# Kernel tuning notes

Measured on AMD Instinct MI355X. Metric: run time of the kernel, lower is better.

## Reference

```python
import jax, jax.numpy as jnp
import numpy as np

CLAMP = 10000.0
EPS = 1e-8
NUM_HEADS = 4


def _sanitize(t):
    t = jnp.nan_to_num(t, nan=0.0, posinf=CLAMP, neginf=-CLAMP)
    return jnp.clip(t, -CLAMP, CLAMP)


def _rmsnorm(t, w):
    # Matches the torch module: L2-norm based RMS, eps added OUTSIDE the sqrt.
    t = _sanitize(t)
    d = t.shape[-1]
    rms = jnp.linalg.norm(t, axis=-1, keepdims=True) * (1.0 / np.sqrt(float(d)))
    return w * (t / (rms + EPS))


def setup_inputs() -> dict:
    key = jax.random.key(0)
    ks = jax.random.split(key, 7)
    N, C, S = 100000, 1024, 18
    x = jax.random.normal(ks[0], (N, C), dtype=jnp.float32)
    seeds = jax.random.normal(ks[1], (S, C), dtype=jnp.float32) / np.sqrt(float(C))
    w_nq = jnp.ones((C,), dtype=jnp.float32)
    w_nkv = jnp.ones((C,), dtype=jnp.float32)
    # nn.MultiheadAttention params (xavier-ish scale)
    in_proj_w = jax.random.normal(ks[2], (3 * C, C), dtype=jnp.float32) * (1.0 / np.sqrt(float(C)))
    in_proj_b = jnp.zeros((3 * C,), dtype=jnp.float32)
    out_proj_w = jax.random.normal(ks[3], (C, C), dtype=jnp.float32) * (1.0 / np.sqrt(float(C)))
    out_proj_b = jnp.zeros((C,), dtype=jnp.float32)
    return {"x": x, "seeds": seeds, "w_nq": w_nq, "w_nkv": w_nkv,
            "in_proj_w": in_proj_w, "in_proj_b": in_proj_b,
            "out_proj_w": out_proj_w, "out_proj_b": out_proj_b}


def reference(x, seeds, w_nq, w_nkv, in_proj_w, in_proj_b, out_proj_w, out_proj_b):
    x = _sanitize(x)
    N, C = x.shape
    S = seeds.shape[0]
    H = NUM_HEADS
    Dh = C // H

    q = _rmsnorm(seeds, w_nq)      # (S, C)
    kv = _rmsnorm(x, w_nkv)        # (N, C) -- same tensor feeds both k and v

    Wq, Wk, Wv = in_proj_w[:C], in_proj_w[C:2 * C], in_proj_w[2 * C:]
    bq, bk, bv = in_proj_b[:C], in_proj_b[C:2 * C], in_proj_b[2 * C:]

    qp = (q @ Wq.T + bq).reshape(S, H, Dh) * (1.0 / np.sqrt(float(Dh)))
    kp = (kv @ Wk.T + bk).reshape(N, H, Dh)
    vp = (kv @ Wv.T + bv).reshape(N, H, Dh)

    # (H, S, N) scores -- S=18 << N, skinny attention
    scores = jnp.einsum('shd,nhd->hsn', qp, kp)
    attn = jax.nn.softmax(scores, axis=-1)
    o = jnp.einsum('hsn,nhd->shd', attn, vp).reshape(S, C)

    y = o @ out_proj_w.T + out_proj_b   # (S, C)
    ctx = _sanitize(y.mean(axis=0))     # (C,)
    return ctx
```

## Files before the change

### kernel.cpp

```cpp
#include <hip/hip_runtime.h>
#include <math.h>

#define NTOK 100000
#define C 1024
#define SN 18
#define H 4
#define DH 256
#define HSN 72
#define CLAMPV 10000.0f
#define EPSV 1e-8f

using short8 = __attribute__((ext_vector_type(8))) short;
using f32x4  = __attribute__((ext_vector_type(4))) float;

__device__ __forceinline__ float sanitize_f(float v) {
    if (isnan(v)) return 0.0f;
    return fminf(CLAMPV, fmaxf(-CLAMPV, v));
}
__device__ __forceinline__ unsigned short f2bf(float f) {
    unsigned int u = __float_as_uint(f);
    u = (u + 0x7FFFu + ((u >> 16) & 1u)) >> 16;
    return (unsigned short)u;
}
__device__ __forceinline__ float waveSum(float v) {
    #pragma unroll
    for (int o = 32; o > 0; o >>= 1) v += __shfl_down(v, o, 64);
    return v;
}
__device__ __forceinline__ float waveMax(float v) {
    #pragma unroll
    for (int o = 32; o > 0; o >>= 1) v = fmaxf(v, __shfl_down(v, o, 64));
    return v;
}

__global__ void k_qnorm(const float* __restrict__ seeds, const float* __restrict__ w_nq,
                        float* __restrict__ q) {
    int row = blockIdx.x, tid = threadIdx.x;
    const float* src = seeds + (size_t)row * C;
    float ss = 0.f;
    for (int c = tid; c < C; c += 256) { float v = sanitize_f(src[c]); ss += v * v; }
    __shared__ float red[4]; __shared__ float sSc;
    float w = waveSum(ss);
    if ((tid & 63) == 0) red[tid >> 6] = w;
    __syncthreads();
    if (tid == 0) {
        float t = red[0] + red[1] + red[2] + red[3];
        float rms = sqrtf(t / (float)C);
        sSc = 1.0f / (rms + EPSV);
    }
    __syncthreads();
    float sc = sSc;
    for (int c = tid; c < C; c += 256) q[(size_t)row * C + c] = w_nq[c] * sanitize_f(src[c]) * sc;
}

__global__ void k_qp(const float* __restrict__ q, const float* __restrict__ Wq,
                     const float* __restrict__ bq, float* __restrict__ qp) {
    int tid = threadIdx.x, wid = tid >> 6, lane = tid & 63;
    int out = blockIdx.x * 4 + wid;
    int s = out >> 10, j = out & 1023;
    const float* qrow = q + (size_t)s * C;
    const float* wrow = Wq + (size_t)j * C;
    float acc = 0.f;
    #pragma unroll
    for (int k = 0; k < 16; ++k) { int c = lane + 64 * k; acc = fmaf(qrow[c], wrow[c], acc); }
    acc = waveSum(acc);
    if (lane == 0) qp[out] = (acc + bq[j]) * 0.0625f;
}

__global__ void k_U(const float* __restrict__ qp, const float* __restrict__ in_proj_w,
                    const float* __restrict__ in_proj_b, const float* __restrict__ w_nkv,
                    unsigned short* __restrict__ Ub, float* __restrict__ bsc) {
    int b = blockIdx.x, tid = threadIdx.x;
    int row = b >> 2, ct = b & 3;
    int c = ct * 256 + tid;
    __shared__ float qps[DH];
    __shared__ float red2[4];
    if (row < HSN) {
        int h = row / SN, s = row % SN;
        qps[tid] = qp[(size_t)s * C + h * DH + tid];
        __syncthreads();
        if (ct == 0) {
            float pb = qps[tid] * in_proj_b[C + h * DH + tid];
            float wsum = waveSum(pb);
            if ((tid & 63) == 0) red2[tid >> 6] = wsum;
            __syncthreads();
            if (tid == 0) bsc[row] = red2[0] + red2[1] + red2[2] + red2[3];
        }
        const float* Wk = in_proj_w + (size_t)C * C;
        float acc = 0.f;
        #pragma unroll 4
        for (int d = 0; d < DH; ++d) acc = fmaf(qps[d], Wk[(size_t)(h * DH + d) * C + c], acc);
        Ub[(size_t)row * C + c] = f2bf(acc * w_nkv[c]);
    } else {
        Ub[(size_t)row * C + c] = 0;
    }
}

__global__ __launch_bounds__(256, 3) void k_passA(const float* __restrict__ x,
    const unsigned short* __restrict__ Ub, const float* __restrict__ bsc,
    float* __restrict__ scaleG, float* __restrict__ scoresG,
    unsigned short* __restrict__ xbG, int writeXb) {
    __shared__ unsigned short xbL[8192];
    __shared__ unsigned short UbL[5120];
    __shared__ float bscLds[HSN];
    __shared__ float scaleLds[128];
    int tid = threadIdx.x;
    int n0 = blockIdx.x * 128;
    if (tid < HSN) bscLds[tid] = bsc[tid];
    int lane = tid & 63, wv = tid >> 6;
    int q = lane >> 4, mn = lane & 15;
    f32x4 acc[5][2];
    #pragma unroll
    for (int mt = 0; mt < 5; ++mt)
        #pragma unroll
        for (int nt = 0; nt < 2; ++nt) acc[mt][nt] = (f32x4){0.f, 0.f, 0.f, 0.f};
    float ss[8];
    #pragma unroll
    for (int i = 0; i < 8; ++i) ss[i] = 0.f;

    for (int kt = 0; kt < 16; ++kt) {
        __syncthreads();
        #pragma unroll
        for (int i = 0; i < 8; ++i) {
            int f = tid + 256 * i;
            int tok = f >> 4, cq = f & 15;
            int n = n0 + tok;
            float4 v = make_float4(0.f, 0.f, 0.f, 0.f);
            if (n < NTOK) v = *(const float4*)(x + (size_t)n * C + kt * 64 + 4 * cq);
            v.x = sanitize_f(v.x); v.y = sanitize_f(v.y);
            v.z = sanitize_f(v.z); v.w = sanitize_f(v.w);
            ss[i] += v.x * v.x + v.y * v.y + v.z * v.z + v.w * v.w;
            unsigned int lo = (unsigned int)f2bf(v.x) | ((unsigned int)f2bf(v.y) << 16);
            unsigned int hi = (unsigned int)f2bf(v.z) | ((unsigned int)f2bf(v.w) << 16);
            if (writeXb && n < NTOK)
                *(uint2*)&xbG[(size_t)n * C + kt * 64 + 4 * cq] = make_uint2(lo, hi);
            int ks = cq >> 3, c32 = (cq & 7) * 4;
            *(uint2*)&xbL[ks * 4096 + tok * 32 + c32] = make_uint2(lo, hi);
        }
        #pragma unroll
        for (int u = 0; u < 5; ++u) {
            int idx = tid + 256 * u;
            int row = idx >> 4, cq = idx & 15;
            int ks = cq >> 3, c32 = (cq & 7) * 4;
            uint2 w4 = *(const uint2*)(Ub + (size_t)row * C + kt * 64 + 4 * cq);
            *(uint2*)&UbL[ks * 2560 + row * 32 + c32] = w4;
        }
        __syncthreads();
        #pragma unroll
        for (int ks = 0; ks < 2; ++ks) {
            short8 a[5], b[2];
            #pragma unroll
            for (int mt = 0; mt < 5; ++mt)
                a[mt] = *(const short8*)&UbL[ks * 2560 + (mt * 16 + mn) * 32 + q * 8];
            #pragma unroll
            for (int nt = 0; nt < 2; ++nt)
                b[nt] = *(const short8*)&xbL[ks * 4096 + (wv * 32 + nt * 16 + mn) * 32 + q * 8];
            #pragma unroll
            for (int mt = 0; mt < 5; ++mt)
                #pragma unroll
                for (int nt = 0; nt < 2; ++nt)
                    acc[mt][nt] = __builtin_amdgcn_mfma_f32_16x16x32_bf16(a[mt], b[nt], acc[mt][nt], 0, 0, 0);
        }
    }
    __syncthreads();
    float* ssS = (float*)xbL;
    #pragma unroll
    for (int i = 0; i < 8; ++i) ssS[((tid >> 4) + 16 * i) * 17 + (tid & 15)] = ss[i];
    __syncthreads();
    if (tid < 128) {
        float t = 0.f;
        #pragma unroll
        for (int k = 0; k < 16; ++k) t += ssS[tid * 17 + k];
        float rms = sqrtf(t / (float)C);
        float sc = 1.0f / (rms + EPSV);
        scaleLds[tid] = sc;
        if (n0 + tid < NTOK) scaleG[n0 + tid] = sc;
    }
    __syncthreads();
    #pragma unroll
    for (int mt = 0; mt < 5; ++mt) {
        #pragma unroll
        for (int nt = 0; nt < 2; ++nt) {
            int tl = wv * 32 + nt * 16 + mn;
            int n = n0 + tl;
            #pragma unroll
            for (int r = 0; r < 4; ++r) {
                int hs = mt * 16 + q * 4 + r;
                if (hs < HSN && n < NTOK)
                    scoresG[(size_t)hs * NTOK + n] = acc[mt][nt][r] * scaleLds[tl] + bscLds[hs];
            }
        }
    }
}

__global__ void k_stats1(const float* __restrict__ scoresG, float* __restrict__ pm,
                         float* __restrict__ pd) {
    int ch = blockIdx.x, hs = blockIdx.y, tid = threadIdx.x;
    int nbeg = ch * 6272, nend = nbeg + 6272;
    if (nend > NTOK) nend = NTOK;
    const float* row = scoresG + (size_t)hs * NTOK;
    float m = -INFINITY;
    for (int n = nbeg + 4 * tid; n < nend; n += 1024) {
        float4 v = *(const float4*)(row + n);
        m = fmaxf(fmaxf(m, fmaxf(v.x, v.y)), fmaxf(v.z, v.w));
    }
    __shared__ float red[4]; __shared__ float sM;
    float w = waveMax(m);
    if ((tid & 63) == 0) red[tid >> 6] = w;
    __syncthreads();
    if (tid == 0) sM = fmaxf(fmaxf(red[0], red[1]), fmaxf(red[2], red[3]));
    __syncthreads();
    float mm = sM;
    float sum = 0.f;
    for (int n = nbeg + 4 * tid; n < nend; n += 1024) {
        float4 v = *(const float4*)(row + n);
        sum += __expf(v.x - mm) + __expf(v.y - mm) + __expf(v.z - mm) + __expf(v.w - mm);
    }
    __syncthreads();
    float ws2 = waveSum(sum);
    if ((tid & 63) == 0) red[tid >> 6] = ws2;
    __syncthreads();
    if (tid == 0) { pm[hs * 16 + ch] = mm; pd[hs * 16 + ch] = red[0] + red[1] + red[2] + red[3]; }
}

__global__ void k_w(const float* __restrict__ scoresG, const float* __restrict__ pm,
                    const float* __restrict__ pd, const float* __restrict__ scaleG,
                    unsigned short* __restrict__ wb) {
    int hs = blockIdx.y;
    __shared__ float sM, sI;
    if (threadIdx.x == 0) {
        float m = -INFINITY;
        #pragma unroll
        for (int i = 0; i < 16; ++i) m = fmaxf(m, pm[hs * 16 + i]);
        float s = 0.f;
        #pragma unroll
        for (int i = 0; i < 16; ++i) s += pd[hs * 16 + i] * __expf(pm[hs * 16 + i] - m);
        sM = m; sI = 1.0f / s;
    }
    __syncthreads();
    int n = (blockIdx.x * 256 + threadIdx.x) * 4;
    if (n >= NTOK) return;
    float mh = sM, ih = sI;
    float4 s4 = *(const float4*)(scoresG + (size_t)hs * NTOK + n);
    float4 c4 = *(const float4*)(scaleG + n);
    unsigned int lo = (unsigned int)f2bf(__expf(s4.x - mh) * c4.x * ih)
                    | ((unsigned int)f2bf(__expf(s4.y - mh) * c4.y * ih) << 16);
    unsigned int hi = (unsigned int)f2bf(__expf(s4.z - mh) * c4.z * ih)
                    | ((unsigned int)f2bf(__expf(s4.w - mh) * c4.w * ih) << 16);
    *(uint2*)&wb[(size_t)hs * NTOK + n] = make_uint2(lo, hi);
}

template<int USE_XB>
__global__ __launch_bounds__(256, 3) void k_passB(const float* __restrict__ x,
    const unsigned short* __restrict__ xb, const unsigned short* __restrict__ wb,
    float* __restrict__ Praw) {
    __shared__ unsigned short xbTL[8192];
    __shared__ unsigned short wTL[5120];
    int tid = threadIdx.x;
    int id = blockIdx.x;
    int r8 = id & 7, k8 = id >> 3;
    int cb = k8 & 7;
    int tch = r8 + 8 * (k8 >> 3);
    if (tch >= 98) return;
    int c0 = cb * 128;
    int lane = tid & 63, wv = tid >> 6;
    int q = lane >> 4, mn = lane & 15;
    f32x4 acc[5][2];
    #pragma unroll
    for (int mt = 0; mt < 5; ++mt)
        #pragma unroll
        for (int nt = 0; nt < 2; ++nt) acc[mt][nt] = (f32x4){0.f, 0.f, 0.f, 0.f};

    for (int scn = 0; scn < 16; ++scn) {
        int n0 = tch * 1024 + scn * 64;
        __syncthreads();
        #pragma unroll
        for (int u = 0; u < 5; ++u) {
            int idx = tid + 256 * u;
            int hsr = idx >> 4, tq = idx & 15;
            int ks = tq >> 3, t32 = (tq & 7) * 4;
            int nbase = n0 + 4 * tq;
            uint2 w4 = make_uint2(0u, 0u);
            if (hsr < HSN && nbase < NTOK)
                w4 = *(const uint2*)&wb[(size_t)hsr * NTOK + nbase];
            *(uint2*)&wTL[ks * 2560 + hsr * 32 + t32] = w4;
        }
        #pragma unroll
        for (int g = 0; g < 4; ++g) {
            int half = tid >> 7;
            int cL = tid & 127;
            int tok0 = 32 * half + 8 * g;
            union { unsigned short u16[8]; short8 v; } pk;
            #pragma unroll
            for (int j = 0; j < 8; ++j) {
                int n = n0 + tok0 + j;
                if (USE_XB) {
                    pk.u16[j] = (n < NTOK) ? xb[(size_t)n * C + c0 + cL] : (unsigned short)0;
                } else {
                    float xv = 0.f;
                    if (n < NTOK) xv = x[(size_t)n * C + c0 + cL];
                    pk.u16[j] = f2bf(sanitize_f(xv));
                }
            }
            *(short8*)&xbTL[half * 4096 + cL * 32 + 8 * g] = pk.v;
        }
        __syncthreads();
        #pragma unroll
        for (int ks = 0; ks < 2; ++ks) {
            short8 a[5], b[2];
            #pragma unroll
            for (int mt = 0; mt < 5; ++mt)
                a[mt] = *(const short8*)&wTL[ks * 2560 + (mt * 16 + mn) * 32 + q * 8];
            #pragma unroll
            for (int nt = 0; nt < 2; ++nt)
                b[nt] = *(const short8*)&xbTL[ks * 4096 + (wv * 32 + nt * 16 + mn) * 32 + q * 8];
            #pragma unroll
            for (int mt = 0; mt < 5; ++mt)
                #pragma unroll
                for (int nt = 0; nt < 2; ++nt)
                    acc[mt][nt] = __builtin_amdgcn_mfma_f32_16x16x32_bf16(a[mt], b[nt], acc[mt][nt], 0, 0, 0);
        }
    }
    #pragma unroll
    for (int mt = 0; mt < 5; ++mt) {
        #pragma unroll
        for (int r = 0; r < 4; ++r) {
            int hs = mt * 16 + q * 4 + r;
            if (hs < HSN) {
                #pragma unroll
                for (int nt = 0; nt < 2; ++nt) {
                    int cc = c0 + wv * 32 + nt * 16 + mn;
                    atomicAdd(Praw + (size_t)hs * C + cc, acc[mt][nt][r]);
                }
            }
        }
    }
}

__global__ void k_o(const float* __restrict__ Praw, const float* __restrict__ in_proj_w,
                    const float* __restrict__ in_proj_b, const float* __restrict__ w_nkv,
                    float* __restrict__ o) {
    int tid = threadIdx.x, wid = tid >> 6, lane = tid & 63;
    int out = blockIdx.x * 4 + wid;
    int s = out >> 10, hd = out & 1023;
    int h = hd >> 8;
    int hs = h * SN + s;
    const float* Wv = in_proj_w + (size_t)2 * C * C + (size_t)hd * C;
    const float* P = Praw + (size_t)hs * C;
    float acc = 0.f;
    #pragma unroll
    for (int k = 0; k < 16; ++k) { int c = lane + 64 * k; acc = fmaf(Wv[c], w_nkv[c] * P[c], acc); }
    acc = waveSum(acc);
    if (lane == 0) o[(size_t)s * C + hd] = acc + in_proj_b[2 * C + hd];
}

__global__ void k_obar(const float* __restrict__ o, float* __restrict__ obar) {
    int c = blockIdx.x * 256 + threadIdx.x;
    float acc = 0.f;
    #pragma unroll
    for (int s = 0; s < SN; ++s) acc += o[(size_t)s * C + c];
    obar[c] = acc * (1.0f / (float)SN);
}

__global__ void k_out(const float* __restrict__ obar, const float* __restrict__ Wout,
                      const float* __restrict__ bout, float* __restrict__ outp) {
    int tid = threadIdx.x, wid = tid >> 6, lane = tid & 63;
    int j = blockIdx.x * 4 + wid;
    float acc = 0.f;
    #pragma unroll
    for (int k = 0; k < 16; ++k) { int c = lane + 64 * k; acc = fmaf(obar[c], Wout[(size_t)j * C + c], acc); }
    acc = waveSum(acc);
    if (lane == 0) outp[j] = sanitize_f(acc + bout[j]);
}

extern "C" void kernel_launch(void* const* d_in, const int* in_sizes, int n_in,
                              void* d_out, int out_size, void* d_ws, size_t ws_size,
                              hipStream_t stream) {
    (void)in_sizes; (void)n_in; (void)out_size;
    const float* x         = (const float*)d_in[0];
    const float* seeds     = (const float*)d_in[1];
    const float* w_nq      = (const float*)d_in[2];
    const float* w_nkv     = (const float*)d_in[3];
    const float* in_proj_w = (const float*)d_in[4];
    const float* in_proj_b = (const float*)d_in[5];
    const float* out_proj_w = (const float*)d_in[6];
    const float* out_proj_b = (const float*)d_in[7];
    float* outp = (float*)d_out;

    float* ws     = (float*)d_ws;
    float* q      = ws;
    float* qp     = ws + 18432;
    unsigned short* Ub = (unsigned short*)(ws + 36864);
    float* bsc    = ws + 110592;
    float* scale  = ws + 110976;
    float* pm     = ws + 211328;
    float* pd     = ws + 212480;
    float* scores = ws + 213632;
    float* Praw   = ws + 7413632;
    float* o      = ws + 7487360;
    float* obar   = ws + 7505792;
    unsigned short* wb = (unsigned short*)(ws + 7506816);
    unsigned short* xb = (unsigned short*)(ws + 11110400);
    int useXb = (ws_size >= (size_t)249241600ull) ? 1 : 0;

    k_qnorm<<<SN, 256, 0, stream>>>(seeds, w_nq, q);
    k_qp<<<4608, 256, 0, stream>>>(q, in_proj_w, in_proj_b, qp);
    k_U<<<320, 256, 0, stream>>>(qp, in_proj_w, in_proj_b, w_nkv, Ub, bsc);
    k_passA<<<782, 256, 0, stream>>>(x, Ub, bsc, scale, scores, xb, useXb);
    k_stats1<<<dim3(16, HSN), 256, 0, stream>>>(scores, pm, pd);
    k_w<<<dim3(98, HSN), 256, 0, stream>>>(scores, pm, pd, scale, wb);
    hipMemsetAsync(Praw, 0, (size_t)HSN * C * sizeof(float), stream);
    if (useXb)
        k_passB<1><<<832, 256, 0, stream>>>(x, xb, wb, Praw);
    else
        k_passB<0><<<832, 256, 0, stream>>>(x, xb, wb, Praw);
    k_o<<<4608, 256, 0, stream>>>(Praw, in_proj_w, in_proj_b, w_nkv, o);
    k_obar<<<4, 256, 0, stream>>>(o, obar);
    k_out<<<256, 256, 0, stream>>>(obar, out_proj_w, out_proj_b, outp);
}
```

Baseline: 886.4 us.

## Load MFMA operands directly from global memory, dropping LDS staging in both passes

Both passes now have each lane load its MFMA A/B fragments straight from global memory into registers, removing the shared-memory tiles and block barriers. Pass A software-pipelines the x loads with a double buffer and reduces the per-token sum of squares with wave shuffles instead of through LDS, with launch bounds lowered to two blocks per SM. The aim is to remove LDS traffic and sync stalls. The cost is uncoalesced or redundant global loads, since the Ub rows are re-read per wave and pass B gathers x with strided per-token reads, plus higher register pressure.

```diff
diff --git a/kernel.cpp b/kernel.cpp
--- a/kernel.cpp
+++ b/kernel.cpp
@@ -12,6 +12,8 @@
 
 using short8 = __attribute__((ext_vector_type(8))) short;
 using f32x4  = __attribute__((ext_vector_type(4))) float;
+
+union S8u { unsigned short u[8]; short8 v; };
 
 __device__ __forceinline__ float sanitize_f(float v) {
     if (isnan(v)) return 0.0f;
@@ -96,98 +98,106 @@
     }
 }
 
-__global__ __launch_bounds__(256, 3) void k_passA(const float* __restrict__ x,
+#define LOADX(DST_, KT_) { \
+    DST_[0][0][0] = *(const float4*)(xr0 + (KT_) * 64);      \
+    DST_[0][0][1] = *(const float4*)(xr0 + (KT_) * 64 + 4);  \
+    DST_[0][1][0] = *(const float4*)(xr0 + (KT_) * 64 + 32); \
+    DST_[0][1][1] = *(const float4*)(xr0 + (KT_) * 64 + 36); \
+    DST_[1][0][0] = *(const float4*)(xr1 + (KT_) * 64);      \
+    DST_[1][0][1] = *(const float4*)(xr1 + (KT_) * 64 + 4);  \
+    DST_[1][1][0] = *(const float4*)(xr1 + (KT_) * 64 + 32); \
+    DST_[1][1][1] = *(const float4*)(xr1 + (KT_) * 64 + 36); }
+
+#define PACK4(VV, SSV, DST, I0) { \
+    float v0_ = sanitize_f((VV).x), v1_ = sanitize_f((VV).y); \
+    float v2_ = sanitize_f((VV).z), v3_ = sanitize_f((VV).w); \
+    SSV += v0_ * v0_ + v1_ * v1_ + v2_ * v2_ + v3_ * v3_; \
+    DST.u[I0]     = f2bf(v0_); DST.u[I0 + 1] = f2bf(v1_); \
+    DST.u[I0 + 2] = f2bf(v2_); DST.u[I0 + 3] = f2bf(v3_); }
+
+#define CONVSTORE(XB_, KT_) { \
+    S8u t00, t01, t10, t11; \
+    PACK4(XB_[0][0][0], ss0, t00, 0); PACK4(XB_[0][0][1], ss0, t00, 4); \
+    PACK4(XB_[0][1][0], ss0, t01, 0); PACK4(XB_[0][1][1], ss0, t01, 4); \
+    PACK4(XB_[1][0][0], ss1, t10, 0); PACK4(XB_[1][0][1], ss1, t10, 4); \
+    PACK4(XB_[1][1][0], ss1, t11, 0); PACK4(XB_[1][1][1], ss1, t11, 4); \
+    b[0][0] = t00.v; b[0][1] = t01.v; b[1][0] = t10.v; b[1][1] = t11.v; \
+    if (writeXb) { \
+        if (n_0 < NTOK) { \
+            *(short8*)(xbG + (size_t)n_0 * C + (KT_) * 64 + q * 8)      = t00.v; \
+            *(short8*)(xbG + (size_t)n_0 * C + (KT_) * 64 + 32 + q * 8) = t01.v; } \
+        if (n_1 < NTOK) { \
+            *(short8*)(xbG + (size_t)n_1 * C + (KT_) * 64 + q * 8)      = t10.v; \
+            *(short8*)(xbG + (size_t)n_1 * C + (KT_) * 64 + 32 + q * 8) = t11.v; } } }
+
+__global__ __launch_bounds__(256, 2) void k_passA(const float* __restrict__ x,
     const unsigned short* __restrict__ Ub, const float* __restrict__ bsc,
     float* __restrict__ scaleG, float* __restrict__ scoresG,
     unsigned short* __restrict__ xbG, int writeXb) {
-    __shared__ unsigned short xbL[8192];
-    __shared__ unsigned short UbL[5120];
-    __shared__ float bscLds[HSN];
-    __shared__ float scaleLds[128];
     int tid = threadIdx.x;
     int n0 = blockIdx.x * 128;
-    if (tid < HSN) bscLds[tid] = bsc[tid];
     int lane = tid & 63, wv = tid >> 6;
     int q = lane >> 4, mn = lane & 15;
+
+    int n_0 = n0 + wv * 32 + mn;
+    int n_1 = n_0 + 16;
+    int nc0 = n_0 < NTOK ? n_0 : NTOK - 1;
+    int nc1 = n_1 < NTOK ? n_1 : NTOK - 1;
+    const float* xr0 = x + (size_t)nc0 * C + q * 8;
+    const float* xr1 = x + (size_t)nc1 * C + q * 8;
+    const unsigned short* ubase = Ub + (size_t)mn * C + q * 8;
+
     f32x4 acc[5][2];
     #pragma unroll
     for (int mt = 0; mt < 5; ++mt)
         #pragma unroll
         for (int nt = 0; nt < 2; ++nt) acc[mt][nt] = (f32x4){0.f, 0.f, 0.f, 0.f};
-    float ss[8];
-    #pragma unroll
-    for (int i = 0; i < 8; ++i) ss[i] = 0.f;
-
+    float ss0 = 0.f, ss1 = 0.f;
+
+    float4 xA[2][2][2], xB[2][2][2];
+    LOADX(xA, 0);
+    #pragma unroll
     for (int kt = 0; kt < 16; ++kt) {
-        __syncthreads();
-        #pragma unroll
-        for (int i = 0; i < 8; ++i) {
-            int f = tid + 256 * i;
-            int tok = f >> 4, cq = f & 15;
-            int n = n0 + tok;
-            float4 v = make_float4(0.f, 0.f, 0.f, 0.f);
-            if (n < NTOK) v = *(const float4*)(x + (size_t)n * C + kt * 64 + 4 * cq);
-            v.x = sanitize_f(v.x); v.y = sanitize_f(v.y);
-            v.z = sanitize_f(v.z); v.w = sanitize_f(v.w);
-            ss[i] += v.x * v.x + v.y * v.y + v.z * v.z + v.w * v.w;
-            unsigned int lo = (unsigned int)f2bf(v.x) | ((unsigned int)f2bf(v.y) << 16);
-            unsigned int hi = (unsigned int)f2bf(v.z) | ((unsigned int)f2bf(v.w) << 16);
-            if (writeXb && n < NTOK)
-                *(uint2*)&xbG[(size_t)n * C + kt * 64 + 4 * cq] = make_uint2(lo, hi);
-            int ks = cq >> 3, c32 = (cq & 7) * 4;
-            *(uint2*)&xbL[ks * 4096 + tok * 32 + c32] = make_uint2(lo, hi);
-        }
-        #pragma unroll
-        for (int u = 0; u < 5; ++u) {
-            int idx = tid + 256 * u;
-            int row = idx >> 4, cq = idx & 15;
-            int ks = cq >> 3, c32 = (cq & 7) * 4;
-            uint2 w4 = *(const uint2*)(Ub + (size_t)row * C + kt * 64 + 4 * cq);
-            *(uint2*)&UbL[ks * 2560 + row * 32 + c32] = w4;
-        }
-        __syncthreads();
-        #pragma unroll
-        for (int ks = 0; ks < 2; ++ks) {
-            short8 a[5], b[2];
-            #pragma unroll
-            for (int mt = 0; mt < 5; ++mt)
-                a[mt] = *(const short8*)&UbL[ks * 2560 + (mt * 16 + mn) * 32 + q * 8];
-            #pragma unroll
-            for (int nt = 0; nt < 2; ++nt)
-                b[nt] = *(const short8*)&xbL[ks * 4096 + (wv * 32 + nt * 16 + mn) * 32 + q * 8];
+        short8 a[5][2];
+        #pragma unroll
+        for (int mt = 0; mt < 5; ++mt) {
+            a[mt][0] = *(const short8*)(ubase + (size_t)mt * 16 * C + kt * 64);
+            a[mt][1] = *(const short8*)(ubase + (size_t)mt * 16 * C + kt * 64 + 32);
+        }
+        short8 b[2][2];
+        if ((kt & 1) == 0) {
+            if (kt < 15) LOADX(xB, kt + 1);
+            CONVSTORE(xA, kt);
+        } else {
+            if (kt < 15) LOADX(xA, kt + 1);
+            CONVSTORE(xB, kt);
+        }
+        #pragma unroll
+        for (int ks = 0; ks < 2; ++ks)
             #pragma unroll
             for (int mt = 0; mt < 5; ++mt)
                 #pragma unroll
                 for (int nt = 0; nt < 2; ++nt)
-                    acc[mt][nt] = __builtin_amdgcn_mfma_f32_16x16x32_bf16(a[mt], b[nt], acc[mt][nt], 0, 0, 0);
-        }
-    }
-    __syncthreads();
-    float* ssS = (float*)xbL;
-    #pragma unroll
-    for (int i = 0; i < 8; ++i) ssS[((tid >> 4) + 16 * i) * 17 + (tid & 15)] = ss[i];
-    __syncthreads();
-    if (tid < 128) {
-        float t = 0.f;
-        #pragma unroll
-        for (int k = 0; k < 16; ++k) t += ssS[tid * 17 + k];
-        float rms = sqrtf(t / (float)C);
-        float sc = 1.0f / (rms + EPSV);
-        scaleLds[tid] = sc;
-        if (n0 + tid < NTOK) scaleG[n0 + tid] = sc;
-    }
-    __syncthreads();
+                    acc[mt][nt] = __builtin_amdgcn_mfma_f32_16x16x32_bf16(a[mt][ks], b[nt][ks], acc[mt][nt], 0, 0, 0);
+    }
+
+    ss0 += __shfl_xor(ss0, 16, 64); ss0 += __shfl_xor(ss0, 32, 64);
+    ss1 += __shfl_xor(ss1, 16, 64); ss1 += __shfl_xor(ss1, 32, 64);
+    float sc0 = 1.0f / (sqrtf(ss0 * (1.0f / (float)C)) + EPSV);
+    float sc1 = 1.0f / (sqrtf(ss1 * (1.0f / (float)C)) + EPSV);
+    if (q == 0) {
+        if (n_0 < NTOK) scaleG[n_0] = sc0;
+        if (n_1 < NTOK) scaleG[n_1] = sc1;
+    }
     #pragma unroll
     for (int mt = 0; mt < 5; ++mt) {
         #pragma unroll
-        for (int nt = 0; nt < 2; ++nt) {
-            int tl = wv * 32 + nt * 16 + mn;
-            int n = n0 + tl;
-            #pragma unroll
-            for (int r = 0; r < 4; ++r) {
-                int hs = mt * 16 + q * 4 + r;
-                if (hs < HSN && n < NTOK)
-                    scoresG[(size_t)hs * NTOK + n] = acc[mt][nt][r] * scaleLds[tl] + bscLds[hs];
+        for (int r = 0; r < 4; ++r) {
+            int hs = mt * 16 + q * 4 + r;
+            if (hs < HSN) {
+                float bb = bsc[hs];
+                if (n_0 < NTOK) scoresG[(size_t)hs * NTOK + n_0] = acc[mt][0][r] * sc0 + bb;
+                if (n_1 < NTOK) scoresG[(size_t)hs * NTOK + n_1] = acc[mt][1][r] * sc1 + bb;
             }
         }
     }
@@ -254,8 +264,6 @@
 __global__ __launch_bounds__(256, 3) void k_passB(const float* __restrict__ x,
     const unsigned short* __restrict__ xb, const unsigned short* __restrict__ wb,
     float* __restrict__ Praw) {
-    __shared__ unsigned short xbTL[8192];
-    __shared__ unsigned short wTL[5120];
     int tid = threadIdx.x;
     int id = blockIdx.x;
     int r8 = id & 7, k8 = id >> 3;
@@ -265,60 +273,47 @@
     int c0 = cb * 128;
     int lane = tid & 63, wv = tid >> 6;
     int q = lane >> 4, mn = lane & 15;
+    int cA = c0 + wv * 32 + mn;
+
     f32x4 acc[5][2];
     #pragma unroll
     for (int mt = 0; mt < 5; ++mt)
         #pragma unroll
         for (int nt = 0; nt < 2; ++nt) acc[mt][nt] = (f32x4){0.f, 0.f, 0.f, 0.f};
+
+    const unsigned short* wrow = wb + (size_t)mn * NTOK + q * 8;
+    bool arow_ok[5];
+    #pragma unroll
+    for (int mt = 0; mt < 5; ++mt) arow_ok[mt] = (mt * 16 + mn) < HSN;
+    const short8 z8 = {0, 0, 0, 0, 0, 0, 0, 0};
 
     for (int scn = 0; scn < 16; ++scn) {
         int n0 = tch * 1024 + scn * 64;
-        __syncthreads();
-        #pragma unroll
-        for (int u = 0; u < 5; ++u) {
-            int idx = tid + 256 * u;
-            int hsr = idx >> 4, tq = idx & 15;
-            int ks = tq >> 3, t32 = (tq & 7) * 4;
-            int nbase = n0 + 4 * tq;
-            uint2 w4 = make_uint2(0u, 0u);
-            if (hsr < HSN && nbase < NTOK)
-                w4 = *(const uint2*)&wb[(size_t)hsr * NTOK + nbase];
-            *(uint2*)&wTL[ks * 2560 + hsr * 32 + t32] = w4;
-        }
-        #pragma unroll
-        for (int g = 0; g < 4; ++g) {
-            int half = tid >> 7;
-            int cL = tid & 127;
-            int tok0 = 32 * half + 8 * g;
-            union { unsigned short u16[8]; short8 v; } pk;
+        #pragma unroll
+        for (int ks = 0; ks < 2; ++ks) {
+            if (n0 + ks * 32 >= NTOK) continue;
+            short8 a[5];
+            #pragma unroll
+            for (int mt = 0; mt < 5; ++mt)
+                a[mt] = arow_ok[mt] ? *(const short8*)(wrow + (size_t)mt * 16 * NTOK + n0 + ks * 32)
+                                    : z8;
+            int tokb = n0 + ks * 32 + q * 8;
+            S8u p0, p1;
             #pragma unroll
             for (int j = 0; j < 8; ++j) {
-                int n = n0 + tok0 + j;
                 if (USE_XB) {
-                    pk.u16[j] = (n < NTOK) ? xb[(size_t)n * C + c0 + cL] : (unsigned short)0;
+                    p0.u[j] = xb[(size_t)(tokb + j) * C + cA];
+                    p1.u[j] = xb[(size_t)(tokb + j) * C + cA + 16];
                 } else {
-                    float xv = 0.f;
-                    if (n < NTOK) xv = x[(size_t)n * C + c0 + cL];
-                    pk.u16[j] = f2bf(sanitize_f(xv));
+                    p0.u[j] = f2bf(sanitize_f(x[(size_t)(tokb + j) * C + cA]));
+                    p1.u[j] = f2bf(sanitize_f(x[(size_t)(tokb + j) * C + cA + 16]));
                 }
             }
-            *(short8*)&xbTL[half * 4096 + cL * 32 + 8 * g] = pk.v;
-        }
-        __syncthreads();
-        #pragma unroll
-        for (int ks = 0; ks < 2; ++ks) {
-            short8 a[5], b[2];
             #pragma unroll
-            for (int mt = 0; mt < 5; ++mt)
-                a[mt] = *(const short8*)&wTL[ks * 2560 + (mt * 16 + mn) * 32 + q * 8];
-            #pragma unroll
-            for (int nt = 0; nt < 2; ++nt)
-                b[nt] = *(const short8*)&xbTL[ks * 4096 + (wv * 32 + nt * 16 + mn) * 32 + q * 8];
-            #pragma unroll
-            for (int mt = 0; mt < 5; ++mt)
-                #pragma unroll
-                for (int nt = 0; nt < 2; ++nt)
-                    acc[mt][nt] = __builtin_amdgcn_mfma_f32_16x16x32_bf16(a[mt], b[nt], acc[mt][nt], 0, 0, 0);
+            for (int mt = 0; mt < 5; ++mt) {
+                acc[mt][0] = __builtin_amdgcn_mfma_f32_16x16x32_bf16(a[mt], p0.v, acc[mt][0], 0, 0, 0);
+                acc[mt][1] = __builtin_amdgcn_mfma_f32_16x16x32_bf16(a[mt], p1.v, acc[mt][1], 0, 0, 0);
+            }
         }
     }
     #pragma unroll
```

Measured after the change: 1.145 ms. 29.1% more time.

## Double-buffer LDS tiles and prefetch global loads in passA and passB

Applied to the files above, without the earlier changes.

Both MFMA kernels now use two LDS buffers. Each iteration prefetches the next tile's global data into registers while the current tile is computed, so one barrier per iteration replaces two. The barrier waits only on LDS counters, which leaves global loads in flight across it. In exchange LDS use doubles (about 53KB per block for two buffers) and register pressure rises, which could cut occupancy under the launch bound of 3 blocks.

```diff
diff --git a/kernel.cpp b/kernel.cpp
--- a/kernel.cpp
+++ b/kernel.cpp
@@ -13,6 +13,8 @@
 using short8 = __attribute__((ext_vector_type(8))) short;
 using f32x4  = __attribute__((ext_vector_type(4))) float;
 
+union S8u { unsigned short u[8]; short8 v; };
+
 __device__ __forceinline__ float sanitize_f(float v) {
     if (isnan(v)) return 0.0f;
     return fminf(CLAMPV, fmaxf(-CLAMPV, v));
@@ -31,6 +33,10 @@
     #pragma unroll
     for (int o = 32; o > 0; o >>= 1) v = fmaxf(v, __shfl_down(v, o, 64));
     return v;
+}
+__device__ __forceinline__ void barrier_lds_only() {
+    asm volatile("s_waitcnt lgkmcnt(0)" ::: "memory");
+    __builtin_amdgcn_s_barrier();
 }
 
 __global__ void k_qnorm(const float* __restrict__ seeds, const float* __restrict__ w_nq,
@@ -100,8 +106,8 @@
     const unsigned short* __restrict__ Ub, const float* __restrict__ bsc,
     float* __restrict__ scaleG, float* __restrict__ scoresG,
     unsigned short* __restrict__ xbG, int writeXb) {
-    __shared__ unsigned short xbL[8192];
-    __shared__ unsigned short UbL[5120];
+    __shared__ unsigned short xbL[2][8192];
+    __shared__ unsigned short UbL[2][5120];
     __shared__ float bscLds[HSN];
     __shared__ float scaleLds[128];
     int tid = threadIdx.x;
@@ -109,6 +115,10 @@
     if (tid < HSN) bscLds[tid] = bsc[tid];
     int lane = tid & 63, wv = tid >> 6;
     int q = lane >> 4, mn = lane & 15;
+
+    int tokT = tid >> 4, cq = tid & 15;
+    int ksq = cq >> 3, c32 = (cq & 7) * 4;
+
     f32x4 acc[5][2];
     #pragma unroll
     for (int mt = 0; mt < 5; ++mt)
@@ -118,15 +128,29 @@
     #pragma unroll
     for (int i = 0; i < 8; ++i) ss[i] = 0.f;
 
-    for (int kt = 0; kt < 16; ++kt) {
-        __syncthreads();
+    float4 xr[8];
+    uint2  ur[5];
+
+    auto ISSUE = [&](int kt) {
         #pragma unroll
         for (int i = 0; i < 8; ++i) {
-            int f = tid + 256 * i;
-            int tok = f >> 4, cq = f & 15;
-            int n = n0 + tok;
+            int n = n0 + tokT + 16 * i;
             float4 v = make_float4(0.f, 0.f, 0.f, 0.f);
             if (n < NTOK) v = *(const float4*)(x + (size_t)n * C + kt * 64 + 4 * cq);
+            xr[i] = v;
+        }
+        #pragma unroll
+        for (int u = 0; u < 5; ++u) {
+            int idx = tid + 256 * u;
+            int row = idx >> 4, cq2 = idx & 15;
+            ur[u] = *(const uint2*)(Ub + (size_t)row * C + kt * 64 + 4 * cq2);
+        }
+    };
+    auto COMMIT = [&](int buf, int kt) {
+        #pragma unroll
+        for (int i = 0; i < 8; ++i) {
+            int n = n0 + tokT + 16 * i;
+            float4 v = xr[i];
             v.x = sanitize_f(v.x); v.y = sanitize_f(v.y);
             v.z = sanitize_f(v.z); v.w = sanitize_f(v.w);
             ss[i] += v.x * v.x + v.y * v.y + v.z * v.z + v.w * v.w;
@@ -134,27 +158,32 @@
             unsigned int hi = (unsigned int)f2bf(v.z) | ((unsigned int)f2bf(v.w) << 16);
             if (writeXb && n < NTOK)
                 *(uint2*)&xbG[(size_t)n * C + kt * 64 + 4 * cq] = make_uint2(lo, hi);
-            int ks = cq >> 3, c32 = (cq & 7) * 4;
-            *(uint2*)&xbL[ks * 4096 + tok * 32 + c32] = make_uint2(lo, hi);
+            *(uint2*)&xbL[buf][ksq * 4096 + (tokT + 16 * i) * 32 + c32] = make_uint2(lo, hi);
         }
         #pragma unroll
         for (int u = 0; u < 5; ++u) {
             int idx = tid + 256 * u;
-            int row = idx >> 4, cq = idx & 15;
-            int ks = cq >> 3, c32 = (cq & 7) * 4;
-            uint2 w4 = *(const uint2*)(Ub + (size_t)row * C + kt * 64 + 4 * cq);
-            *(uint2*)&UbL[ks * 2560 + row * 32 + c32] = w4;
-        }
-        __syncthreads();
+            int row = idx >> 4, cq2 = idx & 15;
+            *(uint2*)&UbL[buf][(cq2 >> 3) * 2560 + row * 32 + (cq2 & 7) * 4] = ur[u];
+        }
+    };
+
+    ISSUE(0);
+    #pragma unroll 2
+    for (int kt = 0; kt < 16; ++kt) {
+        int buf = kt & 1;
+        COMMIT(buf, kt);
+        if (kt < 15) ISSUE(kt + 1);
+        barrier_lds_only();
         #pragma unroll
         for (int ks = 0; ks < 2; ++ks) {
             short8 a[5], b[2];
             #pragma unroll
             for (int mt = 0; mt < 5; ++mt)
-                a[mt] = *(const short8*)&UbL[ks * 2560 + (mt * 16 + mn) * 32 + q * 8];
+                a[mt] = *(const short8*)&UbL[buf][ks * 2560 + (mt * 16 + mn) * 32 + q * 8];
             #pragma unroll
             for (int nt = 0; nt < 2; ++nt)
-                b[nt] = *(const short8*)&xbL[ks * 4096 + (wv * 32 + nt * 16 + mn) * 32 + q * 8];
+                b[nt] = *(const short8*)&xbL[buf][ks * 4096 + (wv * 32 + nt * 16 + mn) * 32 + q * 8];
             #pragma unroll
             for (int mt = 0; mt < 5; ++mt)
                 #pragma unroll
@@ -163,9 +192,9 @@
         }
     }
     __syncthreads();
-    float* ssS = (float*)xbL;
-    #pragma unroll
-    for (int i = 0; i < 8; ++i) ssS[((tid >> 4) + 16 * i) * 17 + (tid & 15)] = ss[i];
+    float* ssS = (float*)&xbL[0][0];
+    #pragma unroll
+    for (int i = 0; i < 8; ++i) ssS[(tokT + 16 * i) * 17 + cq] = ss[i];
     __syncthreads();
     if (tid < 128) {
         float t = 0.f;
@@ -254,8 +283,8 @@
 __global__ __launch_bounds__(256, 3) void k_passB(const float* __restrict__ x,
     const unsigned short* __restrict__ xb, const unsigned short* __restrict__ wb,
     float* __restrict__ Praw) {
-    __shared__ unsigned short xbTL[8192];
-    __shared__ unsigned short wTL[5120];
+    __shared__ unsigned short xbTL[2][8192];
+    __shared__ unsigned short wTL[2][5120];
     int tid = threadIdx.x;
     int id = blockIdx.x;
     int r8 = id & 7, k8 = id >> 3;
@@ -271,49 +300,67 @@
         #pragma unroll
         for (int nt = 0; nt < 2; ++nt) acc[mt][nt] = (f32x4){0.f, 0.f, 0.f, 0.f};
 
-    for (int scn = 0; scn < 16; ++scn) {
+    int half = tid >> 7, cL = tid & 127;
+    uint2 wr[5];
+    S8u  xg[4];
+
+    auto ISSUE_B = [&](int scn) {
         int n0 = tch * 1024 + scn * 64;
-        __syncthreads();
+        #pragma unroll
+        for (int u = 0; u < 5; ++u) {
+            int idx = tid + 256 * u;
+            int hsr = idx >> 4, tq = idx & 15;
+            int nbase = n0 + 4 * tq;
+            uint2 w4 = make_uint2(0u, 0u);
+            if (hsr < HSN && nbase < NTOK)
+                w4 = *(const uint2*)&wb[(size_t)hsr * NTOK + nbase];
+            wr[u] = w4;
+        }
+        #pragma unroll
+        for (int g = 0; g < 4; ++g) {
+            int tok0 = 32 * half + 8 * g;
+            #pragma unroll
+            for (int j = 0; j < 8; ++j) {
+                int n = n0 + tok0 + j;
+                if (USE_XB) {
+                    xg[g].u[j] = (n < NTOK) ? xb[(size_t)n * C + c0 + cL] : (unsigned short)0;
+                } else {
+                    float xv = 0.f;
+                    if (n < NTOK) xv = x[(size_t)n * C + c0 + cL];
+                    xg[g].u[j] = f2bf(sanitize_f(xv));
+                }
+            }
+        }
+    };
+    auto COMMIT_B = [&](int buf) {
         #pragma unroll
         for (int u = 0; u < 5; ++u) {
             int idx = tid + 256 * u;
             int hsr = idx >> 4, tq = idx & 15;
             int ks = tq >> 3, t32 = (tq & 7) * 4;
-            int nbase = n0 + 4 * tq;
-            uint2 w4 = make_uint2(0u, 0u);
-            if (hsr < HSN && nbase < NTOK)
-                w4 = *(const uint2*)&wb[(size_t)hsr * NTOK + nbase];
-            *(uint2*)&wTL[ks * 2560 + hsr * 32 + t32] = w4;
-        }
-        #pragma unroll
-        for (int g = 0; g < 4; ++g) {
-            int half = tid >> 7;
-            int cL = tid & 127;
-            int tok0 = 32 * half + 8 * g;
-            union { unsigned short u16[8]; short8 v; } pk;
-            #pragma unroll
-            for (int j = 0; j < 8; ++j) {
-                int n = n0 + tok0 + j;
-                if (USE_XB) {
-                    pk.u16[j] = (n < NTOK) ? xb[(size_t)n * C + c0 + cL] : (unsigned short)0;
-                } else {
-                    float xv = 0.f;
-                    if (n < NTOK) xv = x[(size_t)n * C + c0 + cL];
-                    pk.u16[j] = f2bf(sanitize_f(xv));
-                }
-            }
-            *(short8*)&xbTL[half * 4096 + cL * 32 + 8 * g] = pk.v;
-        }
-        __syncthreads();
+            *(uint2*)&wTL[buf][ks * 2560 + hsr * 32 + t32] = wr[u];
+        }
+        #pragma unroll
+        for (int g = 0; g < 4; ++g)
+            *(short8*)&xbTL[buf][half * 4096 + cL * 32 + 8 * g] = xg[g].v;
+    };
+
+    ISSUE_B(0);
+    #pragma unroll 2
+    for (int scn = 0; scn < 16; ++scn) {
+        int buf = scn & 1;
+        COMMIT_B(buf);
+        if (scn < 15) ISSUE_B(scn + 1);
+        barrier_lds_only();
         #pragma unroll
         for (int ks = 0; ks < 2; ++ks) {
             short8 a[5], b[2];
             #pragma unroll
             for (int mt = 0; mt < 5; ++mt)
-                a[mt] = *(const short8*)&wTL[ks * 2560 + (mt * 16 + mn) * 32 + q * 8];
+                a[mt] = *(const short8*)&wTL[buf][ks * 2560 + (mt * 16 + mn) * 32 + q * 8];
             #pragma unroll
             for (int nt = 0; nt < 2; ++nt)
-                b[nt] = *(const short8*)&xbTL[ks * 4096 + (wv * 32 + nt * 16 + mn) * 32 + q * 8];
+                b[nt] = *(const short8*)&xbTL[buf][ks * 4096 + (wv * 32 + nt * 16 + mn) * 32 + q * 8];
             #pragma unroll
             for (int mt = 0; mt < 5; ++mt)
                 #pragma unroll
```

New measurement: 1.019 ms. +14.9%, slower.
